# Optimization experiments

Measured on AMD Instinct MI355X. Metric: run time of the kernel, lower is better.

The kernel has to match this reference:

```python
import jax, jax.numpy as jnp
import numpy as np

N_NODES = 50000
N_EDGES = 1600000
IN_SIZE = 256
HIDDEN = 16
HEADS = 8
OUT_SIZE = 16
NEG_SLOPE = 0.2


def setup_inputs() -> dict:
    key = jax.random.key(0)
    ks = jax.random.split(key, 12)
    node_feat = jax.random.normal(ks[0], (N_NODES, IN_SIZE), dtype=jnp.float32)
    src = jax.random.randint(ks[1], (N_EDGES,), 0, N_NODES)
    dst = jax.random.randint(ks[2], (N_EDGES,), 0, N_NODES)
    d1 = HEADS * HIDDEN  # 128
    W1 = jax.random.normal(ks[3], (IN_SIZE, d1), dtype=jnp.float32) / np.sqrt(IN_SIZE)
    al1 = jax.random.normal(ks[4], (HEADS, HIDDEN), dtype=jnp.float32) / np.sqrt(HIDDEN)
    ar1 = jax.random.normal(ks[5], (HEADS, HIDDEN), dtype=jnp.float32) / np.sqrt(HIDDEN)
    b1 = jnp.zeros((d1,), dtype=jnp.float32)
    W2 = jax.random.normal(ks[6], (d1, HEADS * OUT_SIZE), dtype=jnp.float32) / np.sqrt(d1)
    al2 = jax.random.normal(ks[7], (HEADS, OUT_SIZE), dtype=jnp.float32) / np.sqrt(OUT_SIZE)
    ar2 = jax.random.normal(ks[8], (HEADS, OUT_SIZE), dtype=jnp.float32) / np.sqrt(OUT_SIZE)
    b2 = jnp.zeros((HEADS * OUT_SIZE,), dtype=jnp.float32)
    return {"node_feat": node_feat, "src": src, "dst": dst,
            "W1": W1, "al1": al1, "ar1": ar1, "b1": b1,
            "W2": W2, "al2": al2, "ar2": ar2, "b2": b2}


def _gat_conv(h, src, dst, W, attn_l, attn_r, bias, num_nodes):
    """DGL GATConv (eval mode, no dropout, no residual). Returns [N, H, D]."""
    H, D = attn_l.shape
    feat = (h @ W).reshape(-1, H, D)            # [N, H, D]
    el = jnp.sum(feat * attn_l, axis=-1)         # [N, H]
    er = jnp.sum(feat * attn_r, axis=-1)         # [N, H]
    e = jax.nn.leaky_relu(el[src] + er[dst], NEG_SLOPE)   # [E, H]
    # segment softmax over incoming edges of each dst node
    m = jax.ops.segment_max(e, dst, num_segments=num_nodes)
    m = jnp.where(jnp.isfinite(m), m, 0.0)       # guard isolated nodes
    ex = jnp.exp(e - m[dst])
    denom = jax.ops.segment_sum(ex, dst, num_segments=num_nodes)
    alpha = ex / denom[dst]                      # [E, H]
    msg = alpha[:, :, None] * feat[src]          # [E, H, D]
    out = jax.ops.segment_sum(msg, dst, num_segments=num_nodes)  # [N, H, D]
    return out + bias.reshape(H, D)


def reference(node_feat, src, dst, W1, al1, ar1, b1, W2, al2, ar2, b2):
    h = _gat_conv(node_feat, src, dst, W1, al1, ar1, b1, N_NODES)
    h = jax.nn.elu(h).reshape(N_NODES, -1)       # flatten(1) after activation
    out = _gat_conv(h, src, dst, W2, al2, ar2, b2, N_NODES)
    return out.mean(axis=1)                      # mean over heads -> [N, out_size]
```

## Files before the change

kernel.cpp:

```cpp
#include <hip/hip_runtime.h>
#include <hip/hip_bf16.h>

#define N_NODES 50000
#define N_EDGES 1600000
#define HEADS 8
#define HDIM 16
#define D1 128
#define NEG_SLOPE 0.2f
#define RTILES 3125
#define NB 196
#define BCAP 12288
#define B1BLK 320
#define EPB1 5000
#define WPREP_BLKS 217

typedef short short8 __attribute__((ext_vector_type(8)));
typedef float f32x4 __attribute__((ext_vector_type(4)));
typedef _Float16 half8 __attribute__((ext_vector_type(8)));
typedef unsigned char uchar;

__device__ __forceinline__ float bf2f(ushort u) {
    union { unsigned u; float f; } x; x.u = ((unsigned)u) << 16; return x.f;
}
__device__ __forceinline__ ushort f2bf(float f) {
    union { float f; unsigned u; } x; x.f = f;
    unsigned r = x.u + 0x7FFF + ((x.u >> 16) & 1);
    return (ushort)(r >> 16);
}
__device__ __forceinline__ float ldf(const void* p, size_t i, int isf32) {
    return isf32 ? ((const float*)p)[i] : bf2f(((const ushort*)p)[i]);
}
__device__ __forceinline__ void splitbf(float f, ushort& hi, ushort& lo) {
    unsigned u = __float_as_uint(f);
    unsigned uh = u & 0xFFFF0000u;
    hi = (ushort)(uh >> 16);
    lo = f2bf(f - __uint_as_float(uh));
}

#define O_ROWPTR   0
#define O_GCUR     200064
#define O_FLAGS    602240
#define O_ESRC     2202624
#define O_W1HI     5402624
#define O_W1LO     5476352
#define O_W2HI     5550080
#define O_W2LO     5586944
#define O_B1F      5623808
#define O_B2F      5624320
#define O_FEATG    5624832
#define O_EL       18424832
#define O_ER       20024832
#define O_FEATG2   21624832
#define O_EL2      34424832
#define O_ER2      36024832
#define O_PKBUF    O_FEATG2


__global__ __launch_bounds__(256) void k_detect(const ushort* __restrict__ w1, int* __restrict__ flags,
                                                int* __restrict__ gcur) {
    __shared__ int sm[256];
    int t = threadIdx.x;
    if (blockIdx.x == 1) {
        if (t < NB) gcur[t] = 0;
        return;
    }
    int cnt = 0;
    for (int i = t; i < 32768; i += 256) {
        int e = (w1[i] >> 7) & 0xFF;
        if (e >= 0xC8) cnt++;
    }
    sm[t] = cnt; __syncthreads();
    for (int off = 128; off > 0; off >>= 1) {
        if (t < off) sm[t] += sm[t + off];
        __syncthreads();
    }
    if (t == 0) flags[0] = (sm[0] > 0) ? 1 : 0;
}

__device__ __forceinline__ void wprep_elem(const void* W, const void* al, const void* ar,
                                           int K, int kshift, ushort* whi, ushort* wlo,
                                           int isf32, int idx) {
    if (idx >= 144 * K) return;
    int n = idx >> kshift, k = idx & (K - 1);
    float f;
    if (n < 128) {
        f = ldf(W, (size_t)k * 128 + n, isf32);
    } else if (n < 136) {
        int h = n - 128;
        f = 0.f;
#pragma unroll
        for (int d = 0; d < HDIM; ++d)
            f = fmaf(ldf(W, (size_t)k * 128 + h * 16 + d, isf32), ldf(al, h * 16 + d, isf32), f);
    } else {
        int h = n - 136;
        f = 0.f;
#pragma unroll
        for (int d = 0; d < HDIM; ++d)
            f = fmaf(ldf(W, (size_t)k * 128 + h * 16 + d, isf32), ldf(ar, h * 16 + d, isf32), f);
    }
    ushort hi = f2bf(f);
    wlo[n * K + k] = f2bf(f - bf2f(hi));
    whi[n * K + k] = hi;
}

__device__ __forceinline__ void block_scan(int* sm, int t) {
    for (int off = 1; off < 256; off <<= 1) {
        int v = (t >= off) ? sm[t - off] : 0;
        __syncthreads();
        sm[t] += v;
        __syncthreads();
    }
}

#define B1_SMEM 28384

__global__ __launch_bounds__(256) void k_wb1(const void* __restrict__ W1, const void* __restrict__ al1,
                                             const void* __restrict__ ar1, const void* __restrict__ b1,
                                             const void* __restrict__ W2, const void* __restrict__ al2,
                                             const void* __restrict__ ar2, const void* __restrict__ b2,
                                             ushort* __restrict__ w1hi, ushort* __restrict__ w1lo,
                                             ushort* __restrict__ w2hi, ushort* __restrict__ w2lo,
                                             float* __restrict__ b1f, float* __restrict__ b2f,
                                             const int4* __restrict__ src4, const int4* __restrict__ dst4,
                                             int* __restrict__ gcur, uint* __restrict__ pkbuf,
                                             const int* __restrict__ flags) {
    __shared__ __align__(16) char smem[B1_SMEM];
    int b = blockIdx.x, t = threadIdx.x;
    if (b < WPREP_BLKS) {
        int isf32 = flags[0];
        if (b < 144) {
            wprep_elem(W1, al1, ar1, 256, 8, w1hi, w1lo, isf32, b * 256 + t);
        } else if (b < 216) {
            wprep_elem(W2, al2, ar2, 128, 7, w2hi, w2lo, isf32, (b - 144) * 256 + t);
        } else {
            if (t < 128) b1f[t] = ldf(b1, t, isf32);
            else b2f[t - 128] = ldf(b2, t - 128, isf32);
        }
    } else {
        uint*  stage = (uint*)smem;
        uchar* bid   = (uchar*)(smem + 20000);
        uint*  cnt   = (uint*)(smem + 25000);
        int*   loff  = (int*)(smem + 25784);
        int*   goff  = (int*)(smem + 26568);
        int*   sm    = (int*)(smem + 27352);
        int bb = b - WPREP_BLKS;
        for (int w = t; w < NB; w += 256) cnt[w] = 0;
        __syncthreads();
        int base4 = bb * (EPB1 / 4);
        for (int g = t; g < EPB1 / 4; g += 256) {
            int4 d = dst4[base4 + g];
            atomicAdd(&cnt[d.x >> 8], 1u);
            atomicAdd(&cnt[d.y >> 8], 1u);
            atomicAdd(&cnt[d.z >> 8], 1u);
            atomicAdd(&cnt[d.w >> 8], 1u);
        }
        __syncthreads();
        int c = (t < NB) ? (int)cnt[t] : 0;
        sm[t] = c;
        __syncthreads();
        block_scan(sm, t);
        if (t < NB) {
            loff[t] = sm[t] - c;
            goff[t] = atomicAdd(&gcur[t], c);
            cnt[t] = 0;
        }
        __syncthreads();
        for (int g = t; g < EPB1 / 4; g += 256) {
            int4 s = src4[base4 + g];
            int4 d = dst4[base4 + g];
            { int bk = d.x >> 8; int r = atomicAdd(&cnt[bk], 1u); int p = loff[bk] + r; stage[p] = ((uint)s.x << 8) | (uint)(d.x & 255); bid[p] = (uchar)bk; }
            { int bk = d.y >> 8; int r = atomicAdd(&cnt[bk], 1u); int p = loff[bk] + r; stage[p] = ((uint)s.y << 8) | (uint)(d.y & 255); bid[p] = (uchar)bk; }
            { int bk = d.z >> 8; int r = atomicAdd(&cnt[bk], 1u); int p = loff[bk] + r; stage[p] = ((uint)s.z << 8) | (uint)(d.z & 255); bid[p] = (uchar)bk; }
            { int bk = d.w >> 8; int r = atomicAdd(&cnt[bk], 1u); int p = loff[bk] + r; stage[p] = ((uint)s.w << 8) | (uint)(d.w & 255); bid[p] = (uchar)bk; }
        }
        __syncthreads();
        for (int k = t; k < EPB1; k += 256) {
            int bk = (int)bid[k];
            int gi = goff[bk] + (k - loff[bk]);
            if (gi < BCAP) pkbuf[(size_t)bk * BCAP + gi] = stage[k];
        }
    }
}

__device__ __forceinline__ void store_tile(_Float16 (*sfe)[72], _Float16* featg,
                                           const f32x4* acc, int lane, int quad, int l16,
                                           int rowb0, int cbase) {
#pragma unroll
    for (int ci = 0; ci < 4; ++ci)
#pragma unroll
        for (int r = 0; r < 4; ++r)
            sfe[quad * 4 + r][ci * 16 + l16] = (_Float16)acc[ci][r];
    int rr = lane >> 3, ch = lane & 7;
#pragma unroll
    for (int s = 0; s < 2; ++s) {
        int row = s * 8 + rr;
        short8 v = *(const short8*)&sfe[row][ch * 8];
        *(short8*)(featg + (size_t)(rowb0 + row) * D1 + cbase * 16 + ch * 8) = v;
    }
}

__device__ __forceinline__ void gemm1_wave9(const void* A, const ushort* Bhi, const ushort* Blo,
                                            _Float16* featg, float* el, float* er,
                                            int isf32, int rt, int lane, _Float16 (*sfe)[72]) {
    int quad = lane >> 4, l16 = lane & 15;
    const int K = 256;
    size_t a_off = (size_t)(rt * 16 + l16) * K + quad * 8;
    int rowb0 = rt * 16;

    short8 ahi[8], alo[8];
    if (isf32) {
        const float* ap = (const float*)A + a_off;
#pragma unroll
        for (int i = 0; i < 8; ++i) {
            f32x4 u0 = *(const f32x4*)(ap + 32 * i);
            f32x4 u1 = *(const f32x4*)(ap + 32 * i + 4);
            float a8[8] = {u0[0], u0[1], u0[2], u0[3], u1[0], u1[1], u1[2], u1[3]};
#pragma unroll
            for (int j = 0; j < 8; ++j) {
                ushort h, l;
                splitbf(a8[j], h, l);
                ahi[i][j] = (short)h; alo[i][j] = (short)l;
            }
        }
    } else {
        const ushort* ap = (const ushort*)A + a_off;
#pragma unroll
        for (int i = 0; i < 8; ++i) ahi[i] = *(const short8*)(ap + 32 * i);
    }

#pragma unroll
    for (int g = 0; g < 2; ++g) {
        f32x4 acc[4];
#pragma unroll
        for (int ci = 0; ci < 4; ++ci) acc[ci] = (f32x4){0.f, 0.f, 0.f, 0.f};
#pragma unroll
        for (int ci = 0; ci < 4; ++ci) {
            int c = g * 4 + ci;
            const ushort* bh = Bhi + (size_t)(c * 16 + l16) * K + quad * 8;
            if (isf32) {
                const ushort* bl = Blo + (size_t)(c * 16 + l16) * K + quad * 8;
#pragma unroll
                for (int k = 0; k < 8; ++k) {
                    short8 bh8 = *(const short8*)(bh + 32 * k);
                    short8 bl8 = *(const short8*)(bl + 32 * k);
                    acc[ci] = __builtin_amdgcn_mfma_f32_16x16x32_bf16(ahi[k], bh8, acc[ci], 0, 0, 0);
                    acc[ci] = __builtin_amdgcn_mfma_f32_16x16x32_bf16(ahi[k], bl8, acc[ci], 0, 0, 0);
                    acc[ci] = __builtin_amdgcn_mfma_f32_16x16x32_bf16(alo[k], bh8, acc[ci], 0, 0, 0);
                }
            } else {
#pragma unroll
                for (int k = 0; k < 8; ++k) {
                    short8 bh8 = *(const short8*)(bh + 32 * k);
                    acc[ci] = __builtin_amdgcn_mfma_f32_16x16x32_bf16(ahi[k], bh8, acc[ci], 0, 0, 0);
                }
            }
        }
        store_tile(sfe, featg, acc, lane, quad, l16, rowb0, g * 4);
    }

    {
        const ushort* bh = Bhi + (size_t)(8 * 16 + l16) * K + quad * 8;
        const ushort* bl = Blo + (size_t)(8 * 16 + l16) * K + quad * 8;
        f32x4 a = {0.f, 0.f, 0.f, 0.f};
#pragma unroll
        for (int k = 0; k < 8; ++k) {
            short8 bh8 = *(const short8*)(bh + 32 * k);
            short8 bl8 = *(const short8*)(bl + 32 * k);
            a = __builtin_amdgcn_mfma_f32_16x16x32_bf16(ahi[k], bh8, a, 0, 0, 0);
            a = __builtin_amdgcn_mfma_f32_16x16x32_bf16(ahi[k], bl8, a, 0, 0, 0);
            if (isf32) a = __builtin_amdgcn_mfma_f32_16x16x32_bf16(alo[k], bh8, a, 0, 0, 0);
        }
#pragma unroll
        for (int r = 0; r < 4; ++r) {
            int row = rowb0 + quad * 4 + r;
            if (l16 < 8) el[row * 8 + l16] = a[r];
            else         er[row * 8 + (l16 - 8)] = a[r];
        }
    }
}

__global__ __launch_bounds__(256) void k_gemm1(const void* __restrict__ A,
                                               const ushort* __restrict__ w1hi, const ushort* __restrict__ w1lo,
                                               _Float16* __restrict__ featg,
                                               float* __restrict__ el, float* __restrict__ er,
                                               const int* __restrict__ flags) {
    __shared__ __align__(16) _Float16 sfe[4][16][72];
    int wave = threadIdx.x >> 6, lane = threadIdx.x & 63;
    int rt = blockIdx.x * 4 + wave;
    if (rt < RTILES)
        gemm1_wave9(A, w1hi, w1lo, featg, el, er, flags[0], rt, lane, sfe[wave]);
}

__global__ __launch_bounds__(256) void k_bucket2(const uint* __restrict__ pkbuf, const int* __restrict__ gcur,
                                                 ushort* __restrict__ esrc, int* __restrict__ rowptr) {
    __shared__ __align__(16) char smem[76800];
    uint*   pk    = (uint*)smem;
    ushort* es    = (ushort*)(smem + 49152);
    uint*   ncnt  = (uint*)(smem + 73728);
    int*    nbase = (int*)(smem + 74752);
    int*    sm    = (int*)(smem + 75776);
    int b = blockIdx.x, t = threadIdx.x;
    int x = (t < NB) ? gcur[t] : 0;
    sm[t] = x;
    __syncthreads();
    block_scan(sm, t);
    int nb = gcur[b]; if (nb > BCAP) nb = BCAP;
    int bb0 = sm[b] - gcur[b];
    if (b == 0 && t == NB - 1) rowptr[N_NODES] = sm[t];
    __syncthreads();
    ncnt[t] = 0;
    __syncthreads();
    for (int k = t; k < nb; k += 256) {
        uint u = pkbuf[(size_t)b * BCAP + k];
        pk[k] = u;
        atomicAdd(&ncnt[u & 255u], 1u);
    }
    __syncthreads();
    int c = (int)ncnt[t];
    sm[t] = c;
    __syncthreads();
    block_scan(sm, t);
    nbase[t] = sm[t] - c;
    int v = b * 256 + t;
    if (v < N_NODES) rowptr[v] = bb0 + sm[t] - c;
    ncnt[t] = 0;
    __syncthreads();
    for (int k = t; k < nb; k += 256) {
        uint u = pk[k];
        int n = (int)(u & 255u);
        int r = (int)atomicAdd(&ncnt[n], 1u);
        int p = nbase[n] + r;
        if (p < BCAP) es[p] = (ushort)(u >> 8);
    }
    __syncthreads();
    for (int k = t; k < nb; k += 256)
        esrc[bb0 + k] = es[k];
}

__device__ __forceinline__ void gather_wide(const int* __restrict__ rowptr, const ushort* __restrict__ esrc,
                                            const _Float16* __restrict__ featg,
                                            const float* __restrict__ el, const float* __restrict__ er,
                                            int v, int lane, float (&acc)[8], float& den, int& deg) {
    int h8 = lane & 7, esel = lane >> 3;
    int part = lane & 15, a = lane >> 4, hpart = part >> 1;
    float erv = er[v * 8 + h8];
    int beg = rowptr[v], end = rowptr[v + 1];
    deg = end - beg;
#pragma unroll
    for (int c = 0; c < 8; ++c) acc[c] = 0.f;
    den = 0.f;
    for (int j = beg; j < end; j += 8) {
        int nv = end - j;
        int idx = j + h8; if (idx >= end) idx = end - 1;
        int sv = (int)esrc[idx];
        int se = __shfl(sv, esel);
        float x = el[se * 8 + h8] + erv;
        x = x > 0.f ? x : NEG_SLOPE * x;
        float w = __expf(x);
        if (esel >= nv) w = 0.f;
        int s0 = __shfl(sv, a);
        int s1 = __shfl(sv, a + 4);
        half8 g0 = *(const half8*)(featg + (size_t)s0 * 128 + part * 8);
        half8 g1 = *(const half8*)(featg + (size_t)s1 * 128 + part * 8);
        float w0 = __shfl(w, a * 8 + hpart);
        float w1 = __shfl(w, (a + 4) * 8 + hpart);
        den += w0 + w1;
#pragma unroll
        for (int c = 0; c < 8; ++c)
            acc[c] = fmaf(w0, (float)g0[c], fmaf(w1, (float)g1[c], acc[c]));
    }
#pragma unroll
    for (int c = 0; c < 8; ++c) {
        acc[c] += __shfl_xor(acc[c], 16);
        acc[c] += __shfl_xor(acc[c], 32);
    }
    den += __shfl_xor(den, 16);
    den += __shfl_xor(den, 32);
}

__global__ __launch_bounds__(256) void k_agg1m(const int* __restrict__ rowptr, const ushort* __restrict__ esrc,
                                               const _Float16* __restrict__ featg,
                                               const float* __restrict__ el, const float* __restrict__ er,
                                               const float* __restrict__ b1f,
                                               const ushort* __restrict__ w2hi, const ushort* __restrict__ w2lo,
                                               _Float16* __restrict__ featg2,
                                               float* __restrict__ el2, float* __restrict__ er2,
                                               const int* __restrict__ flags) {
    __shared__ __align__(16) ushort sh_hi[16][136];
    __shared__ __align__(16) ushort sh_lo[16][136];
    int isf32 = flags[0];
    int wave = threadIdx.x >> 6, lane = threadIdx.x & 63;
    int part = lane & 15, a = lane >> 4;
    int vb = blockIdx.x * 16;
    f32x4 bia0 = *(const f32x4*)(b1f + part * 8);
    f32x4 bia1 = *(const f32x4*)(b1f + part * 8 + 4);
#pragma unroll
    for (int i = 0; i < 4; ++i) {
        int v = vb + wave * 4 + i;
        float acc[8], den; int dg;
        gather_wide(rowptr, esrc, featg, el, er, v, lane, acc, den, dg);
        float inv = (dg > 0) ? 1.0f / den : 0.f;
        if (a == 0) {
            short8 hi8, lo8;
#pragma unroll
            for (int c = 0; c < 8; ++c) {
                float bc = (c < 4) ? bia0[c] : bia1[c - 4];
                float r = fmaf(acc[c], inv, bc);
                r = r > 0.f ? r : (__expf(r) - 1.f);
                ushort h, l;
                splitbf(r, h, l);
                hi8[c] = (short)h; lo8[c] = (short)l;
            }
            int m = wave * 4 + i;
            *(short8*)&sh_hi[m][part * 8] = hi8;
            *(short8*)&sh_lo[m][part * 8] = lo8;
        }
    }
    __syncthreads();

    int quad = lane >> 4, l16 = lane & 15;
    const int K = 128;
    short8 ahi[4], alo[4];
#pragma unroll
    for (int k = 0; k < 4; ++k) {
        ahi[k] = *(const short8*)&sh_hi[l16][quad * 8 + 32 * k];
        alo[k] = *(const short8*)&sh_lo[l16][quad * 8 + 32 * k];
    }
    int ntile = (wave == 0) ? 3 : 2;
    for (int ti = 0; ti < ntile; ++ti) {
        int c = (ti == 2) ? 8 : wave + ti * 4;
        const ushort* bh = w2hi + (size_t)(c * 16 + l16) * K + quad * 8;
        const ushort* bl = w2lo + (size_t)(c * 16 + l16) * K + quad * 8;
        f32x4 aa = {0.f, 0.f, 0.f, 0.f};
#pragma unroll
        for (int k = 0; k < 4; ++k) {
            short8 bh8 = *(const short8*)(bh + 32 * k);
            aa = __builtin_amdgcn_mfma_f32_16x16x32_bf16(ahi[k], bh8, aa, 0, 0, 0);
            aa = __builtin_amdgcn_mfma_f32_16x16x32_bf16(alo[k], bh8, aa, 0, 0, 0);
            if (c == 8 || isf32) {
                short8 bl8 = *(const short8*)(bl + 32 * k);
                aa = __builtin_amdgcn_mfma_f32_16x16x32_bf16(ahi[k], bl8, aa, 0, 0, 0);
            }
        }
        if (c < 8) {
#pragma unroll
            for (int r = 0; r < 4; ++r)
                featg2[(size_t)(vb + quad * 4 + r) * D1 + c * 16 + l16] = (_Float16)aa[r];
        } else {
#pragma unroll
            for (int r = 0; r < 4; ++r) {
                int row = vb + quad * 4 + r;
                if (l16 < 8) el2[row * 8 + l16] = aa[r];
                else         er2[row * 8 + (l16 - 8)] = aa[r];
            }
        }
    }
}

__global__ __launch_bounds__(256) void k_agg2(const int* __restrict__ rowptr, const ushort* __restrict__ esrc,
                                              const _Float16* __restrict__ featg2,
                                              const float* __restrict__ el2, const float* __restrict__ er2,
                                              const float* __restrict__ b2f,
                                              void* __restrict__ out, const int* __restrict__ flags) {
    int wave = threadIdx.x >> 6, lane = threadIdx.x & 63;
    int v = blockIdx.x * 4 + wave;
    if (v >= N_NODES) return;
    int part = lane & 15;
    float acc[8], den; int dg;
    gather_wide(rowptr, esrc, featg2, el2, er2, v, lane, acc, den, dg);
    float inv = (dg > 0) ? 1.0f / den : 0.f;
    f32x4 bia0 = *(const f32x4*)(b2f + part * 8);
    f32x4 bia1 = *(const f32x4*)(b2f + part * 8 + 4);
    float r[8];
#pragma unroll
    for (int c = 0; c < 8; ++c) {
        float bc = (c < 4) ? bia0[c] : bia1[c - 4];
        r[c] = fmaf(acc[c], inv, bc);
    }
#pragma unroll
    for (int c = 0; c < 8; ++c) {
        r[c] += __shfl_xor(r[c], 2);
        r[c] += __shfl_xor(r[c], 4);
        r[c] += __shfl_xor(r[c], 8);
        r[c] *= 0.125f;
    }
    if (lane < 2) {
        if (flags[0]) {
            float* op = (float*)out + (size_t)v * 16 + lane * 8;
            f32x4 o0 = {r[0], r[1], r[2], r[3]};
            f32x4 o1 = {r[4], r[5], r[6], r[7]};
            *(f32x4*)op = o0;
            *(f32x4*)(op + 4) = o1;
        } else {
            short8 pk;
#pragma unroll
            for (int c = 0; c < 8; ++c) pk[c] = (short)f2bf(r[c]);
            *(short8*)((ushort*)out + (size_t)v * 16 + lane * 8) = pk;
        }
    }
}

extern "C" void kernel_launch(void* const* d_in, const int* in_sizes, int n_in,
                              void* d_out, int out_size, void* d_ws, size_t ws_size,
                              hipStream_t stream) {
    const void* node_feat = d_in[0];
    const int4* src4 = (const int4*)d_in[1];
    const int4* dst4 = (const int4*)d_in[2];
    const void* W1 = d_in[3];
    const void* al1 = d_in[4];
    const void* ar1 = d_in[5];
    const void* b1 = d_in[6];
    const void* W2 = d_in[7];
    const void* al2 = d_in[8];
    const void* ar2 = d_in[9];
    const void* b2 = d_in[10];
    char* ws = (char*)d_ws;

    int* rowptr = (int*)(ws + O_ROWPTR);
    int* gcur   = (int*)(ws + O_GCUR);
    int* flags  = (int*)(ws + O_FLAGS);
    ushort* esrc = (ushort*)(ws + O_ESRC);
    uint* pkbuf = (uint*)(ws + O_PKBUF);
    ushort* w1hi = (ushort*)(ws + O_W1HI);
    ushort* w1lo = (ushort*)(ws + O_W1LO);
    ushort* w2hi = (ushort*)(ws + O_W2HI);
    ushort* w2lo = (ushort*)(ws + O_W2LO);
    float* b1f  = (float*)(ws + O_B1F);
    float* b2f  = (float*)(ws + O_B2F);
    _Float16* featg = (_Float16*)(ws + O_FEATG);
    float* el   = (float*)(ws + O_EL);
    float* er   = (float*)(ws + O_ER);
    _Float16* featg2 = (_Float16*)(ws + O_FEATG2);
    float* el2  = (float*)(ws + O_EL2);
    float* er2  = (float*)(ws + O_ER2);

    k_detect<<<2, 256, 0, stream>>>((const ushort*)W1, flags, gcur);
    k_wb1<<<WPREP_BLKS + B1BLK, 256, 0, stream>>>(W1, al1, ar1, b1, W2, al2, ar2, b2,
                                                  w1hi, w1lo, w2hi, w2lo, b1f, b2f,
                                                  src4, dst4, gcur, pkbuf, flags);
    k_gemm1<<<782, 256, 0, stream>>>(node_feat, w1hi, w1lo, featg, el, er, flags);
    k_bucket2<<<NB, 256, 0, stream>>>(pkbuf, gcur, esrc, rowptr);
    k_agg1m<<<N_NODES / 16, 256, 0, stream>>>(rowptr, esrc, featg, el, er, b1f,
                                              w2hi, w2lo, featg2, el2, er2, flags);
    k_agg2<<<(N_NODES + 3) / 4, 256, 0, stream>>>(rowptr, esrc, featg2, el2, er2,
                                                  b2f, d_out, flags);
}
```

Before: 371.7 us.

## Fuse GEMM1 with CSR bucket sort and inline dtype detection into weight prep

Merges the layer-1 GEMM kernel and the second bucketing pass into one launch, with the extra blocks doing the CSR fill alongside the GEMM tiles. Each bucket is now split across two blocks that each own half the node range, which reduces shared memory per block (19 KB vs 76 KB) and allows higher occupancy. The dtype-detection pass moves into each weight-prep block, so the separate detect kernel becomes a tiny zeroing kernel. The cost is that every weight-prep block rescans 32K weight entries, and the split bucket blocks each read the full bucket twice.

After: 351.3 us. -5.5%, faster.

```diff
diff --git a/kernel.cpp b/kernel.cpp
--- a/kernel.cpp
+++ b/kernel.cpp
@@ -13,6 +13,9 @@
 #define B1BLK 320
 #define EPB1 5000
 #define WPREP_BLKS 217
+#define GEMM_BLKS 782
+#define B2BLK 392
+#define B2CAP 8192
 
 typedef short short8 __attribute__((ext_vector_type(8)));
 typedef float f32x4 __attribute__((ext_vector_type(4)));
@@ -56,25 +59,23 @@
 #define O_PKBUF    O_FEATG2
 
 
-__global__ __launch_bounds__(256) void k_detect(const ushort* __restrict__ w1, int* __restrict__ flags,
-                                                int* __restrict__ gcur) {
-    __shared__ int sm[256];
+__global__ __launch_bounds__(256) void k_zero(int* __restrict__ gcur) {
     int t = threadIdx.x;
-    if (blockIdx.x == 1) {
-        if (t < NB) gcur[t] = 0;
-        return;
-    }
+    if (t < NB) gcur[t] = 0;
+}
+
+__device__ __forceinline__ int detect_isf32(const ushort* __restrict__ w1, int* smflag) {
+    int t = threadIdx.x;
+    if (t == 0) *smflag = 0;
+    __syncthreads();
     int cnt = 0;
     for (int i = t; i < 32768; i += 256) {
         int e = (w1[i] >> 7) & 0xFF;
         if (e >= 0xC8) cnt++;
     }
-    sm[t] = cnt; __syncthreads();
-    for (int off = 128; off > 0; off >>= 1) {
-        if (t < off) sm[t] += sm[t + off];
-        __syncthreads();
-    }
-    if (t == 0) flags[0] = (sm[0] > 0) ? 1 : 0;
+    if (cnt > 0) *smflag = 1;
+    __syncthreads();
+    return *smflag;
 }
 
 __device__ __forceinline__ void wprep_elem(const void* W, const void* al, const void* ar,
@@ -123,11 +124,11 @@
                                              float* __restrict__ b1f, float* __restrict__ b2f,
                                              const int4* __restrict__ src4, const int4* __restrict__ dst4,
                                              int* __restrict__ gcur, uint* __restrict__ pkbuf,
-                                             const int* __restrict__ flags) {
+                                             int* __restrict__ flags) {
     __shared__ __align__(16) char smem[B1_SMEM];
     int b = blockIdx.x, t = threadIdx.x;
     if (b < WPREP_BLKS) {
-        int isf32 = flags[0];
+        int isf32 = detect_isf32((const ushort*)W1, (int*)smem);
         if (b < 144) {
             wprep_elem(W1, al1, ar1, 256, 8, w1hi, w1lo, isf32, b * 256 + t);
         } else if (b < 216) {
@@ -135,6 +136,7 @@
         } else {
             if (t < 128) b1f[t] = ldf(b1, t, isf32);
             else b2f[t - 128] = ldf(b2, t - 128, isf32);
+            if (t == 0) flags[0] = isf32;
         }
     } else {
         uint*  stage = (uint*)smem;
@@ -279,62 +281,70 @@
     }
 }
 
-__global__ __launch_bounds__(256) void k_gemm1(const void* __restrict__ A,
-                                               const ushort* __restrict__ w1hi, const ushort* __restrict__ w1lo,
-                                               _Float16* __restrict__ featg,
-                                               float* __restrict__ el, float* __restrict__ er,
-                                               const int* __restrict__ flags) {
-    __shared__ __align__(16) _Float16 sfe[4][16][72];
-    int wave = threadIdx.x >> 6, lane = threadIdx.x & 63;
-    int rt = blockIdx.x * 4 + wave;
-    if (rt < RTILES)
-        gemm1_wave9(A, w1hi, w1lo, featg, el, er, flags[0], rt, lane, sfe[wave]);
-}
-
-__global__ __launch_bounds__(256) void k_bucket2(const uint* __restrict__ pkbuf, const int* __restrict__ gcur,
-                                                 ushort* __restrict__ esrc, int* __restrict__ rowptr) {
-    __shared__ __align__(16) char smem[76800];
-    uint*   pk    = (uint*)smem;
-    ushort* es    = (ushort*)(smem + 49152);
-    uint*   ncnt  = (uint*)(smem + 73728);
-    int*    nbase = (int*)(smem + 74752);
-    int*    sm    = (int*)(smem + 75776);
+#define G1B2_SMEM 19456
+
+__global__ __launch_bounds__(256) void k_g1b2(const void* __restrict__ A,
+                                              const ushort* __restrict__ w1hi, const ushort* __restrict__ w1lo,
+                                              _Float16* __restrict__ featg,
+                                              float* __restrict__ el, float* __restrict__ er,
+                                              const uint* __restrict__ pkbuf, const int* __restrict__ gcur,
+                                              ushort* __restrict__ esrc, int* __restrict__ rowptr,
+                                              const int* __restrict__ flags) {
+    __shared__ __align__(16) char smem[G1B2_SMEM];
     int b = blockIdx.x, t = threadIdx.x;
-    int x = (t < NB) ? gcur[t] : 0;
-    sm[t] = x;
-    __syncthreads();
-    block_scan(sm, t);
-    int nb = gcur[b]; if (nb > BCAP) nb = BCAP;
-    int bb0 = sm[b] - gcur[b];
-    if (b == 0 && t == NB - 1) rowptr[N_NODES] = sm[t];
-    __syncthreads();
-    ncnt[t] = 0;
-    __syncthreads();
-    for (int k = t; k < nb; k += 256) {
-        uint u = pkbuf[(size_t)b * BCAP + k];
-        pk[k] = u;
-        atomicAdd(&ncnt[u & 255u], 1u);
-    }
-    __syncthreads();
-    int c = (int)ncnt[t];
-    sm[t] = c;
-    __syncthreads();
-    block_scan(sm, t);
-    nbase[t] = sm[t] - c;
-    int v = b * 256 + t;
-    if (v < N_NODES) rowptr[v] = bb0 + sm[t] - c;
-    ncnt[t] = 0;
-    __syncthreads();
-    for (int k = t; k < nb; k += 256) {
-        uint u = pk[k];
-        int n = (int)(u & 255u);
-        int r = (int)atomicAdd(&ncnt[n], 1u);
-        int p = nbase[n] + r;
-        if (p < BCAP) es[p] = (ushort)(u >> 8);
-    }
-    __syncthreads();
-    for (int k = t; k < nb; k += 256)
-        esrc[bb0 + k] = es[k];
+    if (b < GEMM_BLKS) {
+        _Float16 (*sfe4)[16][72] = (_Float16(*)[16][72])smem;
+        int wave = t >> 6, lane = t & 63;
+        int rt = b * 4 + wave;
+        if (rt < RTILES)
+            gemm1_wave9(A, w1hi, w1lo, featg, el, er, flags[0], rt, lane, sfe4[wave]);
+    } else {
+        ushort* es    = (ushort*)smem;
+        uint*   ncnt  = (uint*)(smem + 16384);
+        int*    sm    = (int*)(smem + 17408);
+        int*    nbase = (int*)(smem + 18432);
+        int bb = b - GEMM_BLKS;
+        int bk = bb >> 1, half = bb & 1;
+        int x = (t < NB) ? gcur[t] : 0;
+        sm[t] = x;
+        __syncthreads();
+        block_scan(sm, t);
+        int nb = gcur[bk]; if (nb > BCAP) nb = BCAP;
+        int bb0 = sm[bk] - gcur[bk];
+        if (bb == 0 && t == NB - 1) rowptr[N_NODES] = sm[t];
+        __syncthreads();
+        ncnt[t] = 0;
+        __syncthreads();
+        const uint* pbase = pkbuf + (size_t)bk * BCAP;
+        for (int k = t; k < nb; k += 256)
+            atomicAdd(&ncnt[pbase[k] & 255u], 1u);
+        __syncthreads();
+        int c = (int)ncnt[t];
+        sm[t] = c;
+        __syncthreads();
+        block_scan(sm, t);
+        nbase[t] = sm[t] - c;
+        int v = bk * 256 + t;
+        if (v < N_NODES && (t >> 7) == half) rowptr[v] = bb0 + sm[t] - c;
+        ncnt[t] = 0;
+        __syncthreads();
+        int lo = half * 128, hi = lo + 128;
+        int base0 = nbase[lo];
+        for (int k = t; k < nb; k += 256) {
+            uint u = pbase[k];
+            int n = (int)(u & 255u);
+            if (n >= lo && n < hi) {
+                int r = (int)atomicAdd(&ncnt[n], 1u);
+                int p = nbase[n] + r - base0;
+                if (p >= 0 && p < B2CAP) es[p] = (ushort)(u >> 8);
+            }
+        }
+        __syncthreads();
+        int myedges = sm[hi - 1] - base0;
+        if (myedges > B2CAP) myedges = B2CAP;
+        for (int k = t; k < myedges; k += 256)
+            esrc[bb0 + base0 + k] = es[k];
+    }
 }
 
 __device__ __forceinline__ void gather_wide(const int* __restrict__ rowptr, const ushort* __restrict__ esrc,
@@ -534,12 +544,12 @@
     float* el2  = (float*)(ws + O_EL2);
     float* er2  = (float*)(ws + O_ER2);
 
-    k_detect<<<2, 256, 0, stream>>>((const ushort*)W1, flags, gcur);
+    k_zero<<<1, 256, 0, stream>>>(gcur);
     k_wb1<<<WPREP_BLKS + B1BLK, 256, 0, stream>>>(W1, al1, ar1, b1, W2, al2, ar2, b2,
                                                   w1hi, w1lo, w2hi, w2lo, b1f, b2f,
                                                   src4, dst4, gcur, pkbuf, flags);
-    k_gemm1<<<782, 256, 0, stream>>>(node_feat, w1hi, w1lo, featg, el, er, flags);
-    k_bucket2<<<NB, 256, 0, stream>>>(pkbuf, gcur, esrc, rowptr);
+    k_g1b2<<<GEMM_BLKS + B2BLK, 256, 0, stream>>>(node_feat, w1hi, w1lo, featg, el, er,
+                                                  pkbuf, gcur, esrc, rowptr, flags);
     k_agg1m<<<N_NODES / 16, 256, 0, stream>>>(rowptr, esrc, featg, el, er, b1f,
                                               w2hi, w2lo, featg2, el2, er2, flags);
     k_agg2<<<(N_NODES + 3) / 4, 256, 0, stream>>>(rowptr, esrc, featg2, el2, er2,
```
